# Kernel optimization log

Measured on AMD Instinct MI355X. Metric: run time of the kernel, lower is better.

## Reference

```python
import jax, jax.numpy as jnp
import numpy as np

N_NODES = 50000
N_EDGES = 800000
NFEAT, NHID, NCLASS = 256, 64, 2


def _deg_norm(idx, n_nodes, dtype):
    deg = jax.ops.segment_sum(jnp.ones(idx.shape[0], dtype=dtype), idx, num_segments=n_nodes)
    return jax.lax.rsqrt(jnp.maximum(deg, 1.0))


def gcn_layer(x, W, b, src, dst, n_nodes):
    # DGL GraphConv, norm='both': h = D_in^{-1/2} * Agg( D_out^{-1/2} * x ) W + b
    # weight applied before aggregation (in_feats >= out_feats path); math-equivalent.
    norm_src = _deg_norm(src, n_nodes, x.dtype)  # out-degree norm of source nodes
    norm_dst = _deg_norm(dst, n_nodes, x.dtype)  # in-degree norm of dest nodes
    h = (x * norm_src[:, None]) @ W              # [N, out]
    agg = jax.ops.segment_sum(h[src], dst, num_segments=n_nodes)  # gather + scatter-add
    return agg * norm_dst[:, None] + b


def setup_inputs() -> dict:
    key = jax.random.key(0)
    k1, k2, k3, k4, k5, k6, k7 = jax.random.split(key, 7)
    x = jax.random.normal(k1, (N_NODES, NFEAT), dtype=jnp.float32)
    src = jax.random.randint(k2, (N_EDGES,), 0, N_NODES, dtype=jnp.int64)
    dst = jax.random.randint(k3, (N_EDGES,), 0, N_NODES, dtype=jnp.int64)
    # Glorot-style init like DGL GraphConv
    W1 = jax.random.normal(k4, (NFEAT, NHID), dtype=jnp.float32) * (2.0 / (NFEAT + NHID)) ** 0.5
    b1 = jnp.zeros((NHID,), dtype=jnp.float32)
    W2 = jax.random.normal(k5, (NHID, NCLASS), dtype=jnp.float32) * (2.0 / (NHID + NCLASS)) ** 0.5
    b2 = jnp.zeros((NCLASS,), dtype=jnp.float32)
    return {"x": x, "src": src, "dst": dst, "W1": W1, "b1": b1, "W2": W2, "b2": b2}


def reference(x, src, dst, W1, b1, W2, b2):
    h = jax.nn.relu(gcn_layer(x, W1, b1, src, dst, N_NODES))
    # dropout=False -> p=0, no-op
    logits = gcn_layer(h, W2, b2, src, dst, N_NODES)
    return jax.nn.log_softmax(logits, axis=1)
```

## Files before the change

kernel.cpp:

```cpp
#include <hip/hip_runtime.h>
#include <math.h>

#define N_NODES 50000
#define N_EDGES 800000
#define NFEAT 256
#define NHID 64
#define NCLASS 2

#define DB 64
#define NDB 782
#define BCAP 1536
#define EPB 2048
#define NB_EDGE ((N_EDGES + EPB - 1) / EPB)

#define OFF_CURD 0
#define OFF_CURS 800
#define OFF_RB   1600
#define OFF_DEG  51600
#define OFF_NDST 101600
#define OFF_NSRC 151600
#define OFF_W1T  201600
#define OFF_DPK  209792
#define OFF_SV6  1410944
#define OFF_CSR  1711232
#define OFF_HB   2912384
#define OFF_H2   4512384

typedef __attribute__((ext_vector_type(8))) short bf16x8;
typedef __attribute__((ext_vector_type(8))) short short8;
typedef __attribute__((ext_vector_type(4))) float f32x4;

static __device__ __forceinline__ unsigned short f2bf(float f) {
    union { float f; unsigned int u; } v; v.f = f;
    return (unsigned short)((v.u + 0x8000u) >> 16);
}
static __device__ __forceinline__ unsigned int pk2bf(float f0, float f1) {
    union { float f; unsigned int u; } a, b; a.f = f0; b.f = f1;
    return __builtin_amdgcn_perm(b.u + 0x8000u, a.u + 0x8000u, 0x07060302u);
}
static __device__ __forceinline__ float bflo(unsigned int u) {
    union { unsigned int x; float f; } v; v.x = u << 16; return v.f;
}
static __device__ __forceinline__ float bfhi(unsigned int u) {
    union { unsigned int x; float f; } v; v.x = u & 0xffff0000u; return v.f;
}

#define INIT_N (1600 + NFEAT * NHID)
__global__ __launch_bounds__(256) void init_kernel(const float* __restrict__ W1,
                                                   int* __restrict__ cursors,
                                                   unsigned short* __restrict__ w1t) {
    int g = blockIdx.x * 256 + threadIdx.x;
    if (g < 1600) {
        cursors[g] = 0;
    } else if (g < INIT_N) {
        int idx = g - 1600;
        int k = idx >> 6, n = idx & 63;
        w1t[n * NFEAT + k] = f2bf(W1[idx]);
    }
}

__global__ __launch_bounds__(256) void bscatter_kernel(const int* __restrict__ src,
                                                       const int* __restrict__ dst,
                                                       int* __restrict__ cur_d,
                                                       int* __restrict__ cur_s,
                                                       int* __restrict__ dpk,
                                                       unsigned char* __restrict__ sv6) {
    __shared__ int hd[NDB], bd[NDB], cd[NDB], hs[NDB], bs[NDB], cs[NDB];
    int t = threadIdx.x;
    for (int i = t; i < NDB; i += 256) { hd[i] = 0; cd[i] = 0; hs[i] = 0; cs[i] = 0; }
    __syncthreads();
    int base = blockIdx.x * EPB;
    int ls[8], ld[8];
#pragma unroll
    for (int i = 0; i < 8; ++i) {
        int e = base + t + i * 256;
        ls[i] = (e < N_EDGES) ? src[e] : -1;
        ld[i] = (e < N_EDGES) ? dst[e] : -1;
        if (ld[i] >= 0) {
            atomicAdd(&hd[ld[i] >> 6], 1);
            atomicAdd(&hs[ls[i] >> 6], 1);
        }
    }
    __syncthreads();
    for (int i = t; i < NDB; i += 256) {
        if (hd[i]) bd[i] = atomicAdd(&cur_d[i], hd[i]);
        if (hs[i]) bs[i] = atomicAdd(&cur_s[i], hs[i]);
    }
    __syncthreads();
#pragma unroll
    for (int i = 0; i < 8; ++i) {
        if (ld[i] >= 0) {
            int bin = ld[i] >> 6;
            int pos = bd[bin] + atomicAdd(&cd[bin], 1);
            dpk[bin * BCAP + pos] = (ls[i] << 6) | (ld[i] & 63);
            int sbin = ls[i] >> 6;
            int spos = bs[sbin] + atomicAdd(&cs[sbin], 1);
            sv6[sbin * BCAP + spos] = (unsigned char)(ls[i] & 63);
        }
    }
}

union MidShared {
    struct { unsigned short As[64][136]; unsigned short Bs[64][264]; } g;
    struct { int ebuf[BCAP]; int hist4[256]; int hist[64]; int seg[64]; int cur[64]; } d;
    struct { int hist4[256]; } s;
};
__global__ __launch_bounds__(256) void mid_kernel(const int* __restrict__ cur_d,
                                                  const int* __restrict__ cur_s,
                                                  const int* __restrict__ dpk,
                                                  const unsigned char* __restrict__ sv6,
                                                  const float* __restrict__ x,
                                                  const unsigned short* __restrict__ w1t,
                                                  int* __restrict__ row_beg,
                                                  int* __restrict__ degv,
                                                  float* __restrict__ norm_dst,
                                                  float* __restrict__ norm_src,
                                                  int* __restrict__ csr,
                                                  unsigned short* __restrict__ hb) {
    __shared__ MidShared su;
    int t = threadIdx.x;
    int role = blockIdx.x % 3;
    int b = blockIdx.x / 3;

    if (role == 0) {
        su.s.hist4[t] = 0;
        __syncthreads();
        int cnt = cur_s[b];
        int base = b * BCAP;
        int sub = (t & 3) * 64;
        for (int j = t; j < cnt; j += 256) atomicAdd(&su.s.hist4[sub + sv6[base + j]], 1);
        __syncthreads();
        if (t < 64) {
            int gid = b * 64 + t;
            if (gid < N_NODES) {
                int v = su.s.hist4[t] + su.s.hist4[64 + t] + su.s.hist4[128 + t] + su.s.hist4[192 + t];
                norm_src[gid] = rsqrtf(fmaxf((float)v, 1.0f));
            }
        }
    } else if (role == 1) {
        int cnt = cur_d[b];
        int base = b * BCAP;
        if (t < 64) { su.d.hist[t] = 0; su.d.cur[t] = 0; }
        su.d.hist4[t] = 0;
        for (int j = t; j < cnt; j += 256) su.d.ebuf[j] = dpk[base + j];
        __syncthreads();
        int sub = (t & 3) * 64;
        for (int j = t; j < cnt; j += 256) atomicAdd(&su.d.hist4[sub + (su.d.ebuf[j] & 63)], 1);
        __syncthreads();
        if (t < 64) {
            int v = su.d.hist4[t] + su.d.hist4[64 + t] + su.d.hist4[128 + t] + su.d.hist4[192 + t];
            su.d.hist[t] = v;
            su.d.seg[t] = v;
        }
        __syncthreads();
#pragma unroll
        for (int off = 1; off < 64; off <<= 1) {
            int xv = 0;
            if (t < 64 && t >= off) xv = su.d.seg[t - off];
            __syncthreads();
            if (t < 64) su.d.seg[t] += xv;
            __syncthreads();
        }
        if (t < 64) {
            int v = su.d.hist[t];
            int excl = su.d.seg[t] - v;
            int gid = b * 64 + t;
            if (gid < N_NODES) {
                row_beg[gid] = base + excl;
                degv[gid] = v;
                norm_dst[gid] = rsqrtf(fmaxf((float)v, 1.0f));
            }
            su.d.seg[t] = excl;
        }
        __syncthreads();
        for (int j = t; j < cnt; j += 256) {
            int p = su.d.ebuf[j];
            int dlow = p & 63;
            int pos = base + su.d.seg[dlow] + atomicAdd(&su.d.cur[dlow], 1);
            csr[pos] = ((unsigned)p) >> 6;
        }
    } else {
        const int row0 = b * 64;
#pragma unroll
        for (int i = 0; i < 8; ++i) {
            int c = i * 256 + t;
            int n = c >> 5;
            int k8 = (c & 31) * 8;
            *(short8*)(&su.g.Bs[n][k8]) = *(const short8*)(&w1t[n * NFEAT + k8]);
        }
        const int w = t >> 6;
        const int l = t & 63;
        const int m = l & 15;
        const int kq = (l >> 4) * 8;
        const int q = l >> 4;
        f32x4 acc[4] = {{0.f, 0.f, 0.f, 0.f}, {0.f, 0.f, 0.f, 0.f},
                        {0.f, 0.f, 0.f, 0.f}, {0.f, 0.f, 0.f, 0.f}};
#pragma unroll
        for (int half = 0; half < 2; ++half) {
            __syncthreads();
#pragma unroll
            for (int i = 0; i < 8; ++i) {
                int f = i * 256 + t;
                int r = f >> 5;
                int c4 = (f & 31) * 4;
                int grow = row0 + r;
                float4 av = make_float4(0.f, 0.f, 0.f, 0.f);
                if (grow < N_NODES)
                    av = *(const float4*)(&x[(size_t)grow * NFEAT + half * 128 + c4]);
                uint2 o;
                o.x = pk2bf(av.x, av.y);
                o.y = pk2bf(av.z, av.w);
                *(uint2*)(&su.g.As[r][c4]) = o;
            }
            __syncthreads();
#pragma unroll
            for (int c8 = 0; c8 < 4; ++c8) {
                int k0 = c8 * 32 + kq;
                bf16x8 a = *(const bf16x8*)(&su.g.As[w * 16 + m][k0]);
#pragma unroll
                for (int ct = 0; ct < 4; ++ct) {
                    bf16x8 bb = *(const bf16x8*)(&su.g.Bs[ct * 16 + m][half * 128 + k0]);
                    acc[ct] = __builtin_amdgcn_mfma_f32_16x16x32_bf16(a, bb, acc[ct], 0, 0, 0);
                }
            }
        }
#pragma unroll
        for (int reg = 0; reg < 4; ++reg) {
            int r = row0 + w * 16 + q * 4 + reg;
            if (r < N_NODES) {
#pragma unroll
                for (int ct = 0; ct < 4; ++ct)
                    hb[(size_t)r * NHID + ct * 16 + m] = f2bf(acc[ct][reg]);
            }
        }
    }
}

__global__ __launch_bounds__(256) void fused1_kernel(const int* __restrict__ row_beg,
                                                     const int* __restrict__ degv,
                                                     const int* __restrict__ csr,
                                                     const unsigned short* __restrict__ hb,
                                                     const float* __restrict__ norm_dst,
                                                     const float* __restrict__ norm_src,
                                                     const float* __restrict__ b1,
                                                     const float* __restrict__ W2,
                                                     float* __restrict__ h2) {
    int gtid = blockIdx.x * blockDim.x + threadIdx.x;
    int node = gtid >> 6;
    int lane = gtid & 63;
    if (node >= N_NODES) return;
    int e8 = lane >> 3, fg = lane & 7;
    int beg = row_beg[node];
    int end = beg + degv[node];
    float a0 = 0.f, a1 = 0.f, a2 = 0.f, a3 = 0.f, a4 = 0.f, a5 = 0.f, a6 = 0.f, a7 = 0.f;
    for (int j = beg; j < end; j += 16) {
        int j0 = j + e8, j1 = j0 + 8;
        uint4 u0 = make_uint4(0u, 0u, 0u, 0u), u1 = make_uint4(0u, 0u, 0u, 0u);
        float ns0 = 0.f, ns1 = 0.f;
        if (j0 < end) {
            int s = csr[j0];
            ns0 = norm_src[s];
            u0 = *(const uint4*)(&hb[(size_t)s * NHID + fg * 8]);
        }
        if (j1 < end) {
            int s = csr[j1];
            ns1 = norm_src[s];
            u1 = *(const uint4*)(&hb[(size_t)s * NHID + fg * 8]);
        }
        a0 = fmaf(ns0, bflo(u0.x), fmaf(ns1, bflo(u1.x), a0));
        a1 = fmaf(ns0, bfhi(u0.x), fmaf(ns1, bfhi(u1.x), a1));
        a2 = fmaf(ns0, bflo(u0.y), fmaf(ns1, bflo(u1.y), a2));
        a3 = fmaf(ns0, bfhi(u0.y), fmaf(ns1, bfhi(u1.y), a3));
        a4 = fmaf(ns0, bflo(u0.z), fmaf(ns1, bflo(u1.z), a4));
        a5 = fmaf(ns0, bfhi(u0.z), fmaf(ns1, bfhi(u1.z), a5));
        a6 = fmaf(ns0, bflo(u0.w), fmaf(ns1, bflo(u1.w), a6));
        a7 = fmaf(ns0, bfhi(u0.w), fmaf(ns1, bfhi(u1.w), a7));
    }
#pragma unroll
    for (int off = 8; off <= 32; off <<= 1) {
        a0 += __shfl_xor(a0, off, 64);
        a1 += __shfl_xor(a1, off, 64);
        a2 += __shfl_xor(a2, off, 64);
        a3 += __shfl_xor(a3, off, 64);
        a4 += __shfl_xor(a4, off, 64);
        a5 += __shfl_xor(a5, off, 64);
        a6 += __shfl_xor(a6, off, 64);
        a7 += __shfl_xor(a7, off, 64);
    }
    float nd = norm_dst[node], ns = norm_src[node];
    float4 bv0 = *(const float4*)(&b1[fg * 8]);
    float4 bv1 = *(const float4*)(&b1[fg * 8 + 4]);
    float4 w0 = *(const float4*)(&W2[fg * 16 + 0]);
    float4 w1 = *(const float4*)(&W2[fg * 16 + 4]);
    float4 w2v = *(const float4*)(&W2[fg * 16 + 8]);
    float4 w3 = *(const float4*)(&W2[fg * 16 + 12]);
    float h0 = fmaxf(fmaf(a0, nd, bv0.x), 0.f) * ns;
    float h1 = fmaxf(fmaf(a1, nd, bv0.y), 0.f) * ns;
    float h2f = fmaxf(fmaf(a2, nd, bv0.z), 0.f) * ns;
    float h3 = fmaxf(fmaf(a3, nd, bv0.w), 0.f) * ns;
    float h4 = fmaxf(fmaf(a4, nd, bv1.x), 0.f) * ns;
    float h5 = fmaxf(fmaf(a5, nd, bv1.y), 0.f) * ns;
    float h6 = fmaxf(fmaf(a6, nd, bv1.z), 0.f) * ns;
    float h7 = fmaxf(fmaf(a7, nd, bv1.w), 0.f) * ns;
    float p0 = h0 * w0.x + h1 * w0.z + h2f * w1.x + h3 * w1.z +
               h4 * w2v.x + h5 * w2v.z + h6 * w3.x + h7 * w3.z;
    float p1 = h0 * w0.y + h1 * w0.w + h2f * w1.y + h3 * w1.w +
               h4 * w2v.y + h5 * w2v.w + h6 * w3.y + h7 * w3.w;
#pragma unroll
    for (int off = 1; off <= 4; off <<= 1) {
        p0 += __shfl_xor(p0, off, 64);
        p1 += __shfl_xor(p1, off, 64);
    }
    if (lane == 0) *(float2*)(&h2[node * 2]) = make_float2(p0, p1);
}

__global__ void fused2_kernel(const int* __restrict__ row_beg, const int* __restrict__ degv,
                              const int* __restrict__ csr, const float* __restrict__ h2,
                              const float* __restrict__ norm_dst, const float* __restrict__ b2,
                              float* __restrict__ out) {
    int n = blockIdx.x * blockDim.x + threadIdx.x;
    if (n >= N_NODES) return;
    int beg = row_beg[n], end = beg + degv[n];
    float s0 = 0.f, s1 = 0.f;
    for (int j = beg; j < end; ++j) {
        float2 v = *(const float2*)(&h2[csr[j] * 2]);
        s0 += v.x;
        s1 += v.y;
    }
    float nd = norm_dst[n];
    float l0 = fmaf(s0, nd, b2[0]);
    float l1 = fmaf(s1, nd, b2[1]);
    float m = fmaxf(l0, l1);
    float lse = m + logf(expf(l0 - m) + expf(l1 - m));
    *(float2*)(&out[n * 2]) = make_float2(l0 - lse, l1 - lse);
}

extern "C" void kernel_launch(void* const* d_in, const int* in_sizes, int n_in,
                              void* d_out, int out_size, void* d_ws, size_t ws_size,
                              hipStream_t stream) {
    const float* x  = (const float*)d_in[0];
    const int* src  = (const int*)d_in[1];
    const int* dst  = (const int*)d_in[2];
    const float* W1 = (const float*)d_in[3];
    const float* b1 = (const float*)d_in[4];
    const float* W2 = (const float*)d_in[5];
    const float* b2 = (const float*)d_in[6];
    float* out = (float*)d_out;
    float* ws  = (float*)d_ws;
    int*   wsi = (int*)d_ws;

    int*   cur_d    = wsi + OFF_CURD;
    int*   cur_s    = wsi + OFF_CURS;
    int*   row_beg  = wsi + OFF_RB;
    int*   degv     = wsi + OFF_DEG;
    float* norm_dst = ws + OFF_NDST;
    float* norm_src = ws + OFF_NSRC;
    unsigned short* w1t = (unsigned short*)(wsi + OFF_W1T);
    int*   dpk      = wsi + OFF_DPK;
    unsigned char* sv6 = (unsigned char*)(wsi + OFF_SV6);
    int*   csr      = wsi + OFF_CSR;
    unsigned short* hb = (unsigned short*)(wsi + OFF_HB);
    float* h2       = ws + OFF_H2;

    init_kernel<<<(INIT_N + 255) / 256, 256, 0, stream>>>(W1, cur_d, w1t);
    bscatter_kernel<<<NB_EDGE, 256, 0, stream>>>(src, dst, cur_d, cur_s, dpk, sv6);
    mid_kernel<<<NDB * 3, 256, 0, stream>>>(cur_d, cur_s, dpk, sv6, x, w1t,
                                            row_beg, degv, norm_dst, norm_src, csr, hb);
    {
        long long threads = (long long)N_NODES * 64;
        fused1_kernel<<<(int)((threads + 255) / 256), 256, 0, stream>>>(
            row_beg, degv, csr, hb, norm_dst, norm_src, b1, W2, h2);
    }
    fused2_kernel<<<(N_NODES + 255) / 256, 256, 0, stream>>>(row_beg, degv, csr, h2, norm_dst, b2, out);
}
```

Baseline: 184.3 us.

## Pack row offsets with degrees, unroll edge gather, use 16 lanes per node in layer 2

Row begin and degree are now stored together as one int2, so each node needs a single load instead of two. The layer-1 gather now processes 32 edges per iteration instead of 16, putting more independent loads in flight. The W1 tile is loaded per K-half, which shrinks the mid kernel's shared-memory footprint and may allow more blocks per CU. The layer-2 aggregation now uses 16 lanes per node with a shuffle reduction instead of one serial thread per node, which removes the long per-thread edge loops. The costs are higher register pressure in fused1 and extra shuffle work in fused2.

```diff
diff --git a/kernel.cpp b/kernel.cpp
--- a/kernel.cpp
+++ b/kernel.cpp
@@ -15,8 +15,7 @@
 
 #define OFF_CURD 0
 #define OFF_CURS 800
-#define OFF_RB   1600
-#define OFF_DEG  51600
+#define OFF_RBD  1600
 #define OFF_NDST 101600
 #define OFF_NSRC 151600
 #define OFF_W1T  201600
@@ -101,7 +100,7 @@
 }
 
 union MidShared {
-    struct { unsigned short As[64][136]; unsigned short Bs[64][264]; } g;
+    struct { unsigned short As[64][136]; unsigned short Bs[64][136]; } g;
     struct { int ebuf[BCAP]; int hist4[256]; int hist[64]; int seg[64]; int cur[64]; } d;
     struct { int hist4[256]; } s;
 };
@@ -111,8 +110,7 @@
                                                   const unsigned char* __restrict__ sv6,
                                                   const float* __restrict__ x,
                                                   const unsigned short* __restrict__ w1t,
-                                                  int* __restrict__ row_beg,
-                                                  int* __restrict__ degv,
+                                                  int2* __restrict__ rbdeg,
                                                   float* __restrict__ norm_dst,
                                                   float* __restrict__ norm_src,
                                                   int* __restrict__ csr,
@@ -166,8 +164,7 @@
             int excl = su.d.seg[t] - v;
             int gid = b * 64 + t;
             if (gid < N_NODES) {
-                row_beg[gid] = base + excl;
-                degv[gid] = v;
+                rbdeg[gid] = make_int2(base + excl, v);
                 norm_dst[gid] = rsqrtf(fmaxf((float)v, 1.0f));
             }
             su.d.seg[t] = excl;
@@ -181,13 +178,6 @@
         }
     } else {
         const int row0 = b * 64;
-#pragma unroll
-        for (int i = 0; i < 8; ++i) {
-            int c = i * 256 + t;
-            int n = c >> 5;
-            int k8 = (c & 31) * 8;
-            *(short8*)(&su.g.Bs[n][k8]) = *(const short8*)(&w1t[n * NFEAT + k8]);
-        }
         const int w = t >> 6;
         const int l = t & 63;
         const int m = l & 15;
@@ -212,6 +202,13 @@
                 o.y = pk2bf(av.z, av.w);
                 *(uint2*)(&su.g.As[r][c4]) = o;
             }
+#pragma unroll
+            for (int i = 0; i < 4; ++i) {
+                int c = i * 256 + t;
+                int n = c >> 4;
+                int k8 = (c & 15) * 8;
+                *(short8*)(&su.g.Bs[n][k8]) = *(const short8*)(&w1t[n * NFEAT + half * 128 + k8]);
+            }
             __syncthreads();
 #pragma unroll
             for (int c8 = 0; c8 < 4; ++c8) {
@@ -219,7 +216,7 @@
                 bf16x8 a = *(const bf16x8*)(&su.g.As[w * 16 + m][k0]);
 #pragma unroll
                 for (int ct = 0; ct < 4; ++ct) {
-                    bf16x8 bb = *(const bf16x8*)(&su.g.Bs[ct * 16 + m][half * 128 + k0]);
+                    bf16x8 bb = *(const bf16x8*)(&su.g.Bs[ct * 16 + m][k0]);
                     acc[ct] = __builtin_amdgcn_mfma_f32_16x16x32_bf16(a, bb, acc[ct], 0, 0, 0);
                 }
             }
@@ -236,8 +233,7 @@
     }
 }
 
-__global__ __launch_bounds__(256) void fused1_kernel(const int* __restrict__ row_beg,
-                                                     const int* __restrict__ degv,
+__global__ __launch_bounds__(256) void fused1_kernel(const int2* __restrict__ rbdeg,
                                                      const int* __restrict__ csr,
                                                      const unsigned short* __restrict__ hb,
                                                      const float* __restrict__ norm_dst,
@@ -250,13 +246,15 @@
     int lane = gtid & 63;
     if (node >= N_NODES) return;
     int e8 = lane >> 3, fg = lane & 7;
-    int beg = row_beg[node];
-    int end = beg + degv[node];
+    int2 rd = rbdeg[node];
+    int beg = rd.x;
+    int end = beg + rd.y;
     float a0 = 0.f, a1 = 0.f, a2 = 0.f, a3 = 0.f, a4 = 0.f, a5 = 0.f, a6 = 0.f, a7 = 0.f;
-    for (int j = beg; j < end; j += 16) {
-        int j0 = j + e8, j1 = j0 + 8;
+    for (int j = beg; j < end; j += 32) {
+        int j0 = j + e8, j1 = j0 + 8, j2 = j0 + 16, j3 = j0 + 24;
         uint4 u0 = make_uint4(0u, 0u, 0u, 0u), u1 = make_uint4(0u, 0u, 0u, 0u);
-        float ns0 = 0.f, ns1 = 0.f;
+        uint4 u2 = make_uint4(0u, 0u, 0u, 0u), u3 = make_uint4(0u, 0u, 0u, 0u);
+        float ns0 = 0.f, ns1 = 0.f, ns2 = 0.f, ns3 = 0.f;
         if (j0 < end) {
             int s = csr[j0];
             ns0 = norm_src[s];
@@ -267,14 +265,24 @@
             ns1 = norm_src[s];
             u1 = *(const uint4*)(&hb[(size_t)s * NHID + fg * 8]);
         }
-        a0 = fmaf(ns0, bflo(u0.x), fmaf(ns1, bflo(u1.x), a0));
-        a1 = fmaf(ns0, bfhi(u0.x), fmaf(ns1, bfhi(u1.x), a1));
-        a2 = fmaf(ns0, bflo(u0.y), fmaf(ns1, bflo(u1.y), a2));
-        a3 = fmaf(ns0, bfhi(u0.y), fmaf(ns1, bfhi(u1.y), a3));
-        a4 = fmaf(ns0, bflo(u0.z), fmaf(ns1, bflo(u1.z), a4));
-        a5 = fmaf(ns0, bfhi(u0.z), fmaf(ns1, bfhi(u1.z), a5));
-        a6 = fmaf(ns0, bflo(u0.w), fmaf(ns1, bflo(u1.w), a6));
-        a7 = fmaf(ns0, bfhi(u0.w), fmaf(ns1, bfhi(u1.w), a7));
+        if (j2 < end) {
+            int s = csr[j2];
+            ns2 = norm_src[s];
+            u2 = *(const uint4*)(&hb[(size_t)s * NHID + fg * 8]);
+        }
+        if (j3 < end) {
+            int s = csr[j3];
+            ns3 = norm_src[s];
+            u3 = *(const uint4*)(&hb[(size_t)s * NHID + fg * 8]);
+        }
+        a0 = fmaf(ns0, bflo(u0.x), fmaf(ns1, bflo(u1.x), fmaf(ns2, bflo(u2.x), fmaf(ns3, bflo(u3.x), a0))));
+        a1 = fmaf(ns0, bfhi(u0.x), fmaf(ns1, bfhi(u1.x), fmaf(ns2, bfhi(u2.x), fmaf(ns3, bfhi(u3.x), a1))));
+        a2 = fmaf(ns0, bflo(u0.y), fmaf(ns1, bflo(u1.y), fmaf(ns2, bflo(u2.y), fmaf(ns3, bflo(u3.y), a2))));
+        a3 = fmaf(ns0, bfhi(u0.y), fmaf(ns1, bfhi(u1.y), fmaf(ns2, bfhi(u2.y), fmaf(ns3, bfhi(u3.y), a3))));
+        a4 = fmaf(ns0, bflo(u0.z), fmaf(ns1, bflo(u1.z), fmaf(ns2, bflo(u2.z), fmaf(ns3, bflo(u3.z), a4))));
+        a5 = fmaf(ns0, bfhi(u0.z), fmaf(ns1, bfhi(u1.z), fmaf(ns2, bfhi(u2.z), fmaf(ns3, bfhi(u3.z), a5))));
+        a6 = fmaf(ns0, bflo(u0.w), fmaf(ns1, bflo(u1.w), fmaf(ns2, bflo(u2.w), fmaf(ns3, bflo(u3.w), a6))));
+        a7 = fmaf(ns0, bfhi(u0.w), fmaf(ns1, bfhi(u1.w), fmaf(ns2, bfhi(u2.w), fmaf(ns3, bfhi(u3.w), a7))));
     }
 #pragma unroll
     for (int off = 8; off <= 32; off <<= 1) {
@@ -314,25 +322,37 @@
     if (lane == 0) *(float2*)(&h2[node * 2]) = make_float2(p0, p1);
 }
 
-__global__ void fused2_kernel(const int* __restrict__ row_beg, const int* __restrict__ degv,
-                              const int* __restrict__ csr, const float* __restrict__ h2,
-                              const float* __restrict__ norm_dst, const float* __restrict__ b2,
-                              float* __restrict__ out) {
-    int n = blockIdx.x * blockDim.x + threadIdx.x;
+__global__ __launch_bounds__(256) void fused2_kernel(const int2* __restrict__ rbdeg,
+                                                     const int* __restrict__ csr,
+                                                     const float* __restrict__ h2,
+                                                     const float* __restrict__ norm_dst,
+                                                     const float* __restrict__ b2,
+                                                     float* __restrict__ out) {
+    int gtid = blockIdx.x * blockDim.x + threadIdx.x;
+    int n = gtid >> 4;
+    int l16 = gtid & 15;
     if (n >= N_NODES) return;
-    int beg = row_beg[n], end = beg + degv[n];
+    int2 rd = rbdeg[n];
+    int beg = rd.x, end = rd.x + rd.y;
     float s0 = 0.f, s1 = 0.f;
-    for (int j = beg; j < end; ++j) {
+    for (int j = beg + l16; j < end; j += 16) {
         float2 v = *(const float2*)(&h2[csr[j] * 2]);
         s0 += v.x;
         s1 += v.y;
     }
-    float nd = norm_dst[n];
-    float l0 = fmaf(s0, nd, b2[0]);
-    float l1 = fmaf(s1, nd, b2[1]);
-    float m = fmaxf(l0, l1);
-    float lse = m + logf(expf(l0 - m) + expf(l1 - m));
-    *(float2*)(&out[n * 2]) = make_float2(l0 - lse, l1 - lse);
+#pragma unroll
+    for (int off = 1; off <= 8; off <<= 1) {
+        s0 += __shfl_xor(s0, off, 16);
+        s1 += __shfl_xor(s1, off, 16);
+    }
+    if (l16 == 0) {
+        float nd = norm_dst[n];
+        float l0 = fmaf(s0, nd, b2[0]);
+        float l1 = fmaf(s1, nd, b2[1]);
+        float m = fmaxf(l0, l1);
+        float lse = m + logf(expf(l0 - m) + expf(l1 - m));
+        *(float2*)(&out[n * 2]) = make_float2(l0 - lse, l1 - lse);
+    }
 }
 
 extern "C" void kernel_launch(void* const* d_in, const int* in_sizes, int n_in,
@@ -351,8 +371,7 @@
 
     int*   cur_d    = wsi + OFF_CURD;
     int*   cur_s    = wsi + OFF_CURS;
-    int*   row_beg  = wsi + OFF_RB;
-    int*   degv     = wsi + OFF_DEG;
+    int2*  rbdeg    = (int2*)(wsi + OFF_RBD);
     float* norm_dst = ws + OFF_NDST;
     float* norm_src = ws + OFF_NSRC;
     unsigned short* w1t = (unsigned short*)(wsi + OFF_W1T);
@@ -365,11 +384,15 @@
     init_kernel<<<(INIT_N + 255) / 256, 256, 0, stream>>>(W1, cur_d, w1t);
     bscatter_kernel<<<NB_EDGE, 256, 0, stream>>>(src, dst, cur_d, cur_s, dpk, sv6);
     mid_kernel<<<NDB * 3, 256, 0, stream>>>(cur_d, cur_s, dpk, sv6, x, w1t,
-                                            row_beg, degv, norm_dst, norm_src, csr, hb);
+                                            rbdeg, norm_dst, norm_src, csr, hb);
     {
         long long threads = (long long)N_NODES * 64;
         fused1_kernel<<<(int)((threads + 255) / 256), 256, 0, stream>>>(
-            row_beg, degv, csr, hb, norm_dst, norm_src, b1, W2, h2);
-    }
-    fused2_kernel<<<(N_NODES + 255) / 256, 256, 0, stream>>>(row_beg, degv, csr, h2, norm_dst, b2, out);
-}
+            rbdeg, csr, hb, norm_dst, norm_src, b1, W2, h2);
+    }
+    {
+        long long threads = (long long)N_NODES * 16;
+        fused2_kernel<<<(int)((threads + 255) / 256), 256, 0, stream>>>(
+            rbdeg, csr, h2, norm_dst, b2, out);
+    }
+}
```

Measured after the change: 177.9 us. 3.5% less time.
